# Optimization experiments

Measured on AMD Instinct MI355X. Metric: run time of the kernel, lower is better.

The kernel has to match this reference:

```python
import jax, jax.numpy as jnp
import numpy as np

N_NODES = 2048
DEG = 16
D = 4
E = N_NODES * DEG          # undirected edge count
TWO_E = 2 * E


def setup_inputs() -> dict:
    key = jax.random.key(0)
    # unique off-diagonal (row, col) pairs: sample from n*(n-1) index space
    rng = np.random.default_rng(0)
    p = rng.choice(N_NODES * (N_NODES - 1), size=E, replace=False)
    row = p // (N_NODES - 1)
    c = p % (N_NODES - 1)
    col = c + (c >= row)  # skip the diagonal -> no self loops, all pairs unique
    # edge_index: first E are (i->j), second E the reversed (j->i) in same order
    edge_index = jnp.asarray(
        np.stack([np.concatenate([row, col]), np.concatenate([col, row])]),
        dtype=jnp.int64 if jax.config.jax_enable_x64 else jnp.int32,
    )
    maps = jax.random.normal(key, (TWO_E, D, D), dtype=jnp.float32)
    return {"maps": maps, "edge_index": edge_index, "num_nodes": N_NODES}


def reference(maps, edge_index, num_nodes):
    n = num_nodes
    d = maps.shape[1]
    twoE = maps.shape[0]
    e = twoE // 2

    row_all = edge_index[0]
    # R^T R per directed edge  [2E, d, d]
    diag_contrib = jnp.einsum('eki,ekj->eij', maps, maps)
    # scatter-accumulate into per-node diagonal blocks  [n, d, d]
    maps_diag = jax.ops.segment_sum(diag_contrib, row_all, num_segments=n)

    row = edge_index[0, :e]
    col = edge_index[1, :e]
    # R_ij^T R_ji per undirected edge  [E, d, d]
    maps_triu = jnp.einsum('eki,ekj->eij', maps[:e], maps[e:])

    # eval-mode augmentation: identity
    to_inv = maps_diag + jnp.eye(d, dtype=maps.dtype)
    evals, evecs = jnp.linalg.eigh(to_inv)
    inv_root = jnp.clip(evals, 1e-8, None) ** -0.5
    # V diag(l^-1/2) V^T  [n, d, d]
    inv_sqrt = jnp.einsum('nik,nk,njk->nij', evecs, inv_root, evecs)

    maps_triu = inv_sqrt[row] @ maps_triu @ inv_sqrt[col]
    maps_diag = inv_sqrt @ maps_diag @ inv_sqrt
    maps_triu = jnp.clip(maps_triu, -1.0, 1.0)
    maps_diag = jnp.clip(maps_diag, -1.0, 1.0)

    # dense block Laplacian  [n, n, d, d] -> [n*d, n*d]
    L = jnp.zeros((n, n, d, d), dtype=maps.dtype)
    idx = jnp.arange(n)
    L = L.at[idx, idx].set(maps_diag)
    L = L.at[row, col].set(-maps_triu)
    L = L.at[col, row].set(-jnp.swapaxes(maps_triu, 1, 2))
    return L.transpose(0, 2, 1, 3).reshape(n * d, n * d)
```

## Files before the change

kernel.cpp:

```cpp
#include <hip/hip_runtime.h>
#include <math.h>


#define NNODES 2048
#define MAXDEG 96

__global__ void build_lists_kernel(const int* __restrict__ ei,
                                   int* __restrict__ lists,
                                   int* __restrict__ cnts,
                                   int E, int twoE) {
    int e = blockIdx.x * blockDim.x + threadIdx.x;
    if (e >= twoE) return;
    int node = ei[e];
    int nbr = ei[twoE + e];
    int t = (e >= E) ? 1 : 0;
    int u = t ? (e - E) : e;
    int slot = atomicAdd(&cnts[node], 1);
    if (slot < MAXDEG)
        lists[(size_t)node * MAXDEG + slot] = (nbr << 20) | (t << 19) | u;
}

template <int P, int Q>
__device__ __forceinline__ void jrot(float a[4][4], float v[4][4]) {
    float apq = a[P][Q];
    if (fabsf(apq) < 1e-12f) return;
    float theta = (a[Q][Q] - a[P][P]) / (2.0f * apq);
    float t = 1.0f / (fabsf(theta) + sqrtf(theta * theta + 1.0f));
    t = (theta < 0.0f) ? -t : t;
    float c = 1.0f / sqrtf(t * t + 1.0f);
    float s = t * c;
    #pragma unroll
    for (int k = 0; k < 4; ++k) {
        float akp = a[k][P], akq = a[k][Q];
        a[k][P] = c * akp - s * akq;
        a[k][Q] = s * akp + c * akq;
    }
    #pragma unroll
    for (int k = 0; k < 4; ++k) {
        float apk = a[P][k], aqk = a[Q][k];
        a[P][k] = c * apk - s * aqk;
        a[Q][k] = s * apk + c * aqk;
    }
    #pragma unroll
    for (int k = 0; k < 4; ++k) {
        float vkp = v[k][P], vkq = v[k][Q];
        v[k][P] = c * vkp - s * vkq;
        v[k][Q] = s * vkp + c * vkq;
    }
}

__global__ void __launch_bounds__(64)
node_kernel(const float* __restrict__ maps,
            const int* __restrict__ lists,
            const int* __restrict__ cnts,
            float* __restrict__ Smat,
            float* __restrict__ vdiag,
            int E, int n) {
    int node = blockIdx.x * blockDim.x + threadIdx.x;
    if (node >= n) return;
    float g[4][4];
    #pragma unroll
    for (int i = 0; i < 4; ++i)
        #pragma unroll
        for (int j = 0; j < 4; ++j) g[i][j] = 0.0f;
    int cnt = cnts[node];
    if (cnt > MAXDEG) cnt = MAXDEG;
    const int* myl = lists + (size_t)node * MAXDEG;
    #pragma unroll 4
    for (int j = 0; j < cnt; ++j) {
        int entry = myl[j];
        int t = (entry >> 19) & 1;
        int u = entry & 0x7FFF;
        int e = t ? (E + u) : u;
        const float4* mp = reinterpret_cast<const float4*>(maps + (size_t)e * 16);
        float4 q0 = mp[0], q1 = mp[1], q2 = mp[2], q3 = mp[3];
        float m[4][4] = {{q0.x, q0.y, q0.z, q0.w}, {q1.x, q1.y, q1.z, q1.w},
                         {q2.x, q2.y, q2.z, q2.w}, {q3.x, q3.y, q3.z, q3.w}};
        #pragma unroll
        for (int i = 0; i < 4; ++i)
            #pragma unroll
            for (int jj = 0; jj < 4; ++jj)
                g[i][jj] += m[0][i] * m[0][jj] + m[1][i] * m[1][jj] +
                            m[2][i] * m[2][jj] + m[3][i] * m[3][jj];
    }
    float a[4][4], v[4][4];
    #pragma unroll
    for (int i = 0; i < 4; ++i)
        #pragma unroll
        for (int j = 0; j < 4; ++j) {
            a[i][j] = g[i][j] + (i == j ? 1.0f : 0.0f);
            v[i][j] = (i == j) ? 1.0f : 0.0f;
        }
    #pragma unroll
    for (int sweep = 0; sweep < 6; ++sweep) {
        jrot<0, 1>(a, v); jrot<0, 2>(a, v); jrot<0, 3>(a, v);
        jrot<1, 2>(a, v); jrot<1, 3>(a, v); jrot<2, 3>(a, v);
    }
    float ir[4];
    #pragma unroll
    for (int m = 0; m < 4; ++m)
        ir[m] = 1.0f / sqrtf(fmaxf(a[m][m], 1e-8f));
    float s[4][4];
    #pragma unroll
    for (int i = 0; i < 4; ++i)
        #pragma unroll
        for (int j = 0; j < 4; ++j)
            s[i][j] = v[i][0] * v[j][0] * ir[0] + v[i][1] * v[j][1] * ir[1] +
                      v[i][2] * v[j][2] * ir[2] + v[i][3] * v[j][3] * ir[3];
    float4* sp = reinterpret_cast<float4*>(Smat + (size_t)node * 16);
    sp[0] = make_float4(s[0][0], s[0][1], s[0][2], s[0][3]);
    sp[1] = make_float4(s[1][0], s[1][1], s[1][2], s[1][3]);
    sp[2] = make_float4(s[2][0], s[2][1], s[2][2], s[2][3]);
    sp[3] = make_float4(s[3][0], s[3][1], s[3][2], s[3][3]);
    float t1[4][4];
    #pragma unroll
    for (int i = 0; i < 4; ++i)
        #pragma unroll
        for (int j = 0; j < 4; ++j)
            t1[i][j] = s[i][0] * g[0][j] + s[i][1] * g[1][j] +
                       s[i][2] * g[2][j] + s[i][3] * g[3][j];
    float4* vp = reinterpret_cast<float4*>(vdiag + (size_t)node * 16);
    #pragma unroll
    for (int i = 0; i < 4; ++i) {
        float r0 = t1[i][0] * s[0][0] + t1[i][1] * s[1][0] + t1[i][2] * s[2][0] + t1[i][3] * s[3][0];
        float r1 = t1[i][0] * s[0][1] + t1[i][1] * s[1][1] + t1[i][2] * s[2][1] + t1[i][3] * s[3][1];
        float r2 = t1[i][0] * s[0][2] + t1[i][1] * s[1][2] + t1[i][2] * s[2][2] + t1[i][3] * s[3][2];
        float r3 = t1[i][0] * s[0][3] + t1[i][1] * s[1][3] + t1[i][2] * s[2][3] + t1[i][3] * s[3][3];
        vp[i] = make_float4(fminf(fmaxf(r0, -1.0f), 1.0f),
                            fminf(fmaxf(r1, -1.0f), 1.0f),
                            fminf(fmaxf(r2, -1.0f), 1.0f),
                            fminf(fmaxf(r3, -1.0f), 1.0f));
    }
}

__global__ void __launch_bounds__(256)
writer_kernel(const float* __restrict__ maps,
              const int* __restrict__ lists,
              const int* __restrict__ cnts,
              const float* __restrict__ Smat,
              const float* __restrict__ vdiag,
              float* __restrict__ out, int E, int ld) {
    int r = blockIdx.x;
    int tid = threadIdx.x;
    __shared__ int colmap[NNODES];
    __shared__ float4 s_dat[MAXDEG + 1][4];
    for (int i = tid; i < NNODES; i += 256) colmap[i] = -1;

    int cnt = cnts[r];
    if (cnt > MAXDEG) cnt = MAXDEG;
    int col = -1, t = 0;
    if (tid < cnt) {
        int entry = lists[(size_t)r * MAXDEG + tid];
        col = entry >> 20;
        t = (entry >> 19) & 1;
        int u = entry & 0x7FFF;
        const float4* ap = reinterpret_cast<const float4*>(maps + (size_t)u * 16);
        const float4* bp = reinterpret_cast<const float4*>(maps + (size_t)(E + u) * 16);
        float4 a0 = ap[0], a1 = ap[1], a2 = ap[2], a3 = ap[3];
        float4 b0 = bp[0], b1 = bp[1], b2 = bp[2], b3 = bp[3];
        float A[4][4] = {{a0.x, a0.y, a0.z, a0.w}, {a1.x, a1.y, a1.z, a1.w},
                         {a2.x, a2.y, a2.z, a2.w}, {a3.x, a3.y, a3.z, a3.w}};
        float B[4][4] = {{b0.x, b0.y, b0.z, b0.w}, {b1.x, b1.y, b1.z, b1.w},
                         {b2.x, b2.y, b2.z, b2.w}, {b3.x, b3.y, b3.z, b3.w}};
        float C[4][4];
        #pragma unroll
        for (int i = 0; i < 4; ++i)
            #pragma unroll
            for (int j = 0; j < 4; ++j)
                C[i][j] = A[0][i] * B[0][j] + A[1][i] * B[1][j] +
                          A[2][i] * B[2][j] + A[3][i] * B[3][j];
        int rn = t ? col : r;
        int cn = t ? r : col;
        const float4* srp = reinterpret_cast<const float4*>(Smat + (size_t)rn * 16);
        const float4* scp = reinterpret_cast<const float4*>(Smat + (size_t)cn * 16);
        float4 s0 = srp[0], s1 = srp[1], s2 = srp[2], s3 = srp[3];
        float Sr[4][4] = {{s0.x, s0.y, s0.z, s0.w}, {s1.x, s1.y, s1.z, s1.w},
                          {s2.x, s2.y, s2.z, s2.w}, {s3.x, s3.y, s3.z, s3.w}};
        float4 c0 = scp[0], c1 = scp[1], c2 = scp[2], c3 = scp[3];
        float Sc[4][4] = {{c0.x, c0.y, c0.z, c0.w}, {c1.x, c1.y, c1.z, c1.w},
                          {c2.x, c2.y, c2.z, c2.w}, {c3.x, c3.y, c3.z, c3.w}};
        float t1m[4][4];
        #pragma unroll
        for (int i = 0; i < 4; ++i)
            #pragma unroll
            for (int j = 0; j < 4; ++j)
                t1m[i][j] = Sr[i][0] * C[0][j] + Sr[i][1] * C[1][j] +
                            Sr[i][2] * C[2][j] + Sr[i][3] * C[3][j];
        float W[4][4];
        #pragma unroll
        for (int i = 0; i < 4; ++i)
            #pragma unroll
            for (int j = 0; j < 4; ++j) {
                float x = t1m[i][0] * Sc[0][j] + t1m[i][1] * Sc[1][j] +
                          t1m[i][2] * Sc[2][j] + t1m[i][3] * Sc[3][j];
                W[i][j] = -fminf(fmaxf(x, -1.0f), 1.0f);
            }
        if (t) {
            s_dat[tid][0] = make_float4(W[0][0], W[1][0], W[2][0], W[3][0]);
            s_dat[tid][1] = make_float4(W[0][1], W[1][1], W[2][1], W[3][1]);
            s_dat[tid][2] = make_float4(W[0][2], W[1][2], W[2][2], W[3][2]);
            s_dat[tid][3] = make_float4(W[0][3], W[1][3], W[2][3], W[3][3]);
        } else {
            s_dat[tid][0] = make_float4(W[0][0], W[0][1], W[0][2], W[0][3]);
            s_dat[tid][1] = make_float4(W[1][0], W[1][1], W[1][2], W[1][3]);
            s_dat[tid][2] = make_float4(W[2][0], W[2][1], W[2][2], W[2][3]);
            s_dat[tid][3] = make_float4(W[3][0], W[3][1], W[3][2], W[3][3]);
        }
    }
    if (tid < 4)
        s_dat[MAXDEG][tid] = reinterpret_cast<const float4*>(vdiag + (size_t)r * 16)[tid];
    __syncthreads();
    if (tid < cnt && !t) colmap[col] = tid;
    __syncthreads();
    if (tid < cnt && t) colmap[col] = tid;
    if (tid == 0) colmap[r] = MAXDEG;
    __syncthreads();

    size_t base = (size_t)(r * 4) * (size_t)ld;
    const float4 zero = make_float4(0.f, 0.f, 0.f, 0.f);
    #pragma unroll
    for (int ri = 0; ri < 4; ++ri) {
        float4* orow = reinterpret_cast<float4*>(out + base + (size_t)ri * ld);
        for (int cb = tid; cb < NNODES; cb += 256) {
            int sl = colmap[cb];
            float4 val = zero;
            if (sl >= 0) val = s_dat[sl][ri];
            orow[cb] = val;
        }
    }
}

extern "C" void kernel_launch(void* const* d_in, const int* in_sizes, int n_in,
                              void* d_out, int out_size, void* d_ws, size_t ws_size,
                              hipStream_t stream) {
    const float* maps = (const float*)d_in[0];
    const int* ei = (const int*)d_in[1];
    int twoE = in_sizes[0] / 16;
    int E = twoE / 2;
    const int n = NNODES;
    const int ld = n * 4;
    float* out = (float*)d_out;

    int*   ws_cnt  = (int*)d_ws;
    int*   ws_list = ws_cnt + n;
    float* ws_S    = (float*)(ws_list + (size_t)n * MAXDEG);
    float* ws_vd   = ws_S + (size_t)n * 16;

    hipMemsetAsync(ws_cnt, 0, (size_t)n * sizeof(int), stream);

    build_lists_kernel<<<(twoE + 255) / 256, 256, 0, stream>>>(ei, ws_list, ws_cnt, E, twoE);
    node_kernel<<<(n + 63) / 64, 64, 0, stream>>>(maps, ws_list, ws_cnt, ws_S, ws_vd, E, n);
    writer_kernel<<<n, 256, 0, stream>>>(maps, ws_list, ws_cnt, ws_S, ws_vd, out, E, ld);
}
```

Baseline: 94.85 us.

## Fuse memset, list build, node and writer stages into one cooperative kernel

Replaces the memset plus three kernel launches with a single cooperative persistent kernel that uses grid-wide syncs between the count reset, adjacency-list build, per-node eigen/inverse-sqrt stage and the dense row writer. The aim is to remove launch gaps and inter-kernel drain overhead. In exchange, the node stage runs on only a fraction of threads, the grid is capped by occupancy (assuming 256 CUs), and grid syncs add their own cost. The original multi-kernel path is kept as a fallback if the cooperative launch fails.

```diff
diff --git a/kernel.cpp b/kernel.cpp
--- a/kernel.cpp
+++ b/kernel.cpp
@@ -1,24 +1,13 @@
 #include <hip/hip_runtime.h>
+#include <hip/hip_cooperative_groups.h>
 #include <math.h>
+
+namespace cg = cooperative_groups;
 
 
 #define NNODES 2048
 #define MAXDEG 96
-
-__global__ void build_lists_kernel(const int* __restrict__ ei,
-                                   int* __restrict__ lists,
-                                   int* __restrict__ cnts,
-                                   int E, int twoE) {
-    int e = blockIdx.x * blockDim.x + threadIdx.x;
-    if (e >= twoE) return;
-    int node = ei[e];
-    int nbr = ei[twoE + e];
-    int t = (e >= E) ? 1 : 0;
-    int u = t ? (e - E) : e;
-    int slot = atomicAdd(&cnts[node], 1);
-    if (slot < MAXDEG)
-        lists[(size_t)node * MAXDEG + slot] = (nbr << 20) | (t << 19) | u;
-}
+#define BLK 256
 
 template <int P, int Q>
 __device__ __forceinline__ void jrot(float a[4][4], float v[4][4]) {
@@ -49,20 +38,18 @@
     }
 }
 
-__global__ void __launch_bounds__(64)
-node_kernel(const float* __restrict__ maps,
-            const int* __restrict__ lists,
-            const int* __restrict__ cnts,
-            float* __restrict__ Smat,
-            float* __restrict__ vdiag,
-            int E, int n) {
-    int node = blockIdx.x * blockDim.x + threadIdx.x;
-    if (node >= n) return;
-    float g[4][4];
+__device__ __forceinline__ void node_work(int node,
+                                          const float* __restrict__ maps,
+                                          const int* __restrict__ lists,
+                                          const int* __restrict__ cnts,
+                                          float* __restrict__ Smat,
+                                          float* __restrict__ vdiag,
+                                          int E) {
+    float gm[4][4];
     #pragma unroll
     for (int i = 0; i < 4; ++i)
         #pragma unroll
-        for (int j = 0; j < 4; ++j) g[i][j] = 0.0f;
+        for (int j = 0; j < 4; ++j) gm[i][j] = 0.0f;
     int cnt = cnts[node];
     if (cnt > MAXDEG) cnt = MAXDEG;
     const int* myl = lists + (size_t)node * MAXDEG;
@@ -80,15 +67,15 @@
         for (int i = 0; i < 4; ++i)
             #pragma unroll
             for (int jj = 0; jj < 4; ++jj)
-                g[i][jj] += m[0][i] * m[0][jj] + m[1][i] * m[1][jj] +
-                            m[2][i] * m[2][jj] + m[3][i] * m[3][jj];
+                gm[i][jj] += m[0][i] * m[0][jj] + m[1][i] * m[1][jj] +
+                             m[2][i] * m[2][jj] + m[3][i] * m[3][jj];
     }
     float a[4][4], v[4][4];
     #pragma unroll
     for (int i = 0; i < 4; ++i)
         #pragma unroll
         for (int j = 0; j < 4; ++j) {
-            a[i][j] = g[i][j] + (i == j ? 1.0f : 0.0f);
+            a[i][j] = gm[i][j] + (i == j ? 1.0f : 0.0f);
             v[i][j] = (i == j) ? 1.0f : 0.0f;
         }
     #pragma unroll
@@ -117,8 +104,8 @@
     for (int i = 0; i < 4; ++i)
         #pragma unroll
         for (int j = 0; j < 4; ++j)
-            t1[i][j] = s[i][0] * g[0][j] + s[i][1] * g[1][j] +
-                       s[i][2] * g[2][j] + s[i][3] * g[3][j];
+            t1[i][j] = s[i][0] * gm[0][j] + s[i][1] * gm[1][j] +
+                       s[i][2] * gm[2][j] + s[i][3] * gm[3][j];
     float4* vp = reinterpret_cast<float4*>(vdiag + (size_t)node * 16);
     #pragma unroll
     for (int i = 0; i < 4; ++i) {
@@ -133,18 +120,16 @@
     }
 }
 
-__global__ void __launch_bounds__(256)
-writer_kernel(const float* __restrict__ maps,
-              const int* __restrict__ lists,
-              const int* __restrict__ cnts,
-              const float* __restrict__ Smat,
-              const float* __restrict__ vdiag,
-              float* __restrict__ out, int E, int ld) {
-    int r = blockIdx.x;
-    int tid = threadIdx.x;
-    __shared__ int colmap[NNODES];
-    __shared__ float4 s_dat[MAXDEG + 1][4];
-    for (int i = tid; i < NNODES; i += 256) colmap[i] = -1;
+__device__ __forceinline__ void row_work(int r, int tid,
+                                         const float* __restrict__ maps,
+                                         const int* __restrict__ lists,
+                                         const int* __restrict__ cnts,
+                                         const float* __restrict__ Smat,
+                                         const float* __restrict__ vdiag,
+                                         float* __restrict__ out,
+                                         int E, int ld,
+                                         int* colmap, float4 (*s_dat)[4]) {
+    for (int i = tid; i < NNODES; i += BLK) colmap[i] = -1;
 
     int cnt = cnts[r];
     if (cnt > MAXDEG) cnt = MAXDEG;
@@ -208,7 +193,8 @@
         }
     }
     if (tid < 4)
-        s_dat[MAXDEG][tid] = reinterpret_cast<const float4*>(vdiag + (size_t)r * 16)[tid];
+        s_dat[MAXDEG][tid] =
+            reinterpret_cast<const float4*>(vdiag + (size_t)r * 16)[tid];
     __syncthreads();
     if (tid < cnt && !t) colmap[col] = tid;
     __syncthreads();
@@ -221,13 +207,95 @@
     #pragma unroll
     for (int ri = 0; ri < 4; ++ri) {
         float4* orow = reinterpret_cast<float4*>(out + base + (size_t)ri * ld);
-        for (int cb = tid; cb < NNODES; cb += 256) {
+        for (int cb = tid; cb < NNODES; cb += BLK) {
             int sl = colmap[cb];
             float4 val = zero;
             if (sl >= 0) val = s_dat[sl][ri];
             orow[cb] = val;
         }
     }
+}
+
+__global__ void __launch_bounds__(BLK, 2)
+fused_kernel(const float* __restrict__ maps,
+             const int* __restrict__ ei,
+             int* __restrict__ lists,
+             int* __restrict__ cnts,
+             float* __restrict__ Smat,
+             float* __restrict__ vdiag,
+             float* __restrict__ out,
+             int E, int twoE, int n, int ld) {
+    cg::grid_group gg = cg::this_grid();
+    const int tid = threadIdx.x;
+    const int gid = blockIdx.x;
+    const int g = gid * BLK + tid;
+    const int gstride = gridDim.x * BLK;
+
+    for (int i = g; i < n; i += gstride) cnts[i] = 0;
+    gg.sync();
+
+    for (int e = g; e < twoE; e += gstride) {
+        int node = ei[e];
+        int nbr = ei[twoE + e];
+        int t = (e >= E) ? 1 : 0;
+        int u = t ? (e - E) : e;
+        int slot = atomicAdd(&cnts[node], 1);
+        if (slot < MAXDEG)
+            lists[(size_t)node * MAXDEG + slot] = (nbr << 20) | (t << 19) | u;
+    }
+    gg.sync();
+
+    for (int node = g; node < n; node += gstride)
+        node_work(node, maps, lists, cnts, Smat, vdiag, E);
+    gg.sync();
+
+    __shared__ int colmap[NNODES];
+    __shared__ float4 s_dat[MAXDEG + 1][4];
+    for (int r = gid; r < n; r += gridDim.x) {
+        row_work(r, tid, maps, lists, cnts, Smat, vdiag, out, E, ld,
+                 colmap, s_dat);
+        __syncthreads();
+    }
+}
+
+__global__ void build_lists_kernel(const int* __restrict__ ei,
+                                   int* __restrict__ lists,
+                                   int* __restrict__ cnts,
+                                   int E, int twoE) {
+    int e = blockIdx.x * blockDim.x + threadIdx.x;
+    if (e >= twoE) return;
+    int node = ei[e];
+    int nbr = ei[twoE + e];
+    int t = (e >= E) ? 1 : 0;
+    int u = t ? (e - E) : e;
+    int slot = atomicAdd(&cnts[node], 1);
+    if (slot < MAXDEG)
+        lists[(size_t)node * MAXDEG + slot] = (nbr << 20) | (t << 19) | u;
+}
+
+__global__ void __launch_bounds__(64)
+node_kernel(const float* __restrict__ maps,
+            const int* __restrict__ lists,
+            const int* __restrict__ cnts,
+            float* __restrict__ Smat,
+            float* __restrict__ vdiag,
+            int E, int n) {
+    int node = blockIdx.x * blockDim.x + threadIdx.x;
+    if (node >= n) return;
+    node_work(node, maps, lists, cnts, Smat, vdiag, E);
+}
+
+__global__ void __launch_bounds__(BLK)
+writer_kernel(const float* __restrict__ maps,
+              const int* __restrict__ lists,
+              const int* __restrict__ cnts,
+              const float* __restrict__ Smat,
+              const float* __restrict__ vdiag,
+              float* __restrict__ out, int E, int ld) {
+    __shared__ int colmap[NNODES];
+    __shared__ float4 s_dat[MAXDEG + 1][4];
+    row_work(blockIdx.x, threadIdx.x, maps, lists, cnts, Smat, vdiag, out,
+             E, ld, colmap, s_dat);
 }
 
 extern "C" void kernel_launch(void* const* d_in, const int* in_sizes, int n_in,
@@ -237,8 +305,8 @@
     const int* ei = (const int*)d_in[1];
     int twoE = in_sizes[0] / 16;
     int E = twoE / 2;
-    const int n = NNODES;
-    const int ld = n * 4;
+    int n = NNODES;
+    int ld = n * 4;
     float* out = (float*)d_out;
 
     int*   ws_cnt  = (int*)d_ws;
@@ -246,9 +314,35 @@
     float* ws_S    = (float*)(ws_list + (size_t)n * MAXDEG);
     float* ws_vd   = ws_S + (size_t)n * 16;
 
-    hipMemsetAsync(ws_cnt, 0, (size_t)n * sizeof(int), stream);
-
-    build_lists_kernel<<<(twoE + 255) / 256, 256, 0, stream>>>(ei, ws_list, ws_cnt, E, twoE);
-    node_kernel<<<(n + 63) / 64, 64, 0, stream>>>(maps, ws_list, ws_cnt, ws_S, ws_vd, E, n);
-    writer_kernel<<<n, 256, 0, stream>>>(maps, ws_list, ws_cnt, ws_S, ws_vd, out, E, ld);
-}
+    bool coop_done = false;
+    int occ = 0;
+    hipError_t qrc = hipOccupancyMaxActiveBlocksPerMultiprocessor(
+        &occ, fused_kernel, BLK, 0);
+    if (qrc == hipSuccess && occ > 0) {
+        int grid = occ * 256;
+        if (grid > NNODES) grid = NNODES;
+        void* args[] = {(void*)&maps, (void*)&ei, (void*)&ws_list,
+                        (void*)&ws_cnt, (void*)&ws_S, (void*)&ws_vd,
+                        (void*)&out, (void*)&E, (void*)&twoE,
+                        (void*)&n, (void*)&ld};
+        hipError_t rc = hipLaunchCooperativeKernel(
+            (const void*)fused_kernel, dim3(grid), dim3(BLK), args, 0, stream);
+        if (rc == hipSuccess) {
+            coop_done = true;
+        } else {
+            (void)hipGetLastError();
+        }
+    } else {
+        (void)hipGetLastError();
+    }
+
+    if (!coop_done) {
+        hipMemsetAsync(ws_cnt, 0, (size_t)n * sizeof(int), stream);
+        build_lists_kernel<<<(twoE + BLK - 1) / BLK, BLK, 0, stream>>>(
+            ei, ws_list, ws_cnt, E, twoE);
+        node_kernel<<<(n + 63) / 64, 64, 0, stream>>>(
+            maps, ws_list, ws_cnt, ws_S, ws_vd, E, n);
+        writer_kernel<<<n, BLK, 0, stream>>>(
+            maps, ws_list, ws_cnt, ws_S, ws_vd, out, E, ld);
+    }
+}
```

Result: slower. 240.4 us (+153.5%).
